# Performance work log

Hardware: AMD Instinct MI355X
Metric: run time of the kernel (lower is better)

The kernel has to match this reference:

```python
import jax, jax.numpy as jnp
import numpy as np

MAP_CHANNEL_WEIGHT = 50.0
PATCH = 3  # unfold kernel size and stride (stride == kernel -> non-overlapping)


def setup_inputs() -> dict:
    key = jax.random.key(0)
    k1, k2, k3, k4 = jax.random.split(key, 4)
    style_resp = jax.random.normal(k1, (1, 256, 256, 256), dtype=jnp.float32)
    style_map = jax.random.uniform(k2, (1, 3, 1024, 1024), dtype=jnp.float32)
    output_map = jax.random.uniform(k3, (1, 3, 1024, 1024), dtype=jnp.float32)
    model_resp = jax.random.normal(k4, (1, 256, 256, 256), dtype=jnp.float32)
    return {"style_resp": style_resp, "style_map": style_map,
            "output_map": output_map, "model_resp": model_resp}


def _avg_pool(x, d):
    # x: (N, C, H, W) -> AvgPool2d((d, d)) with default stride = kernel
    n, c, h, w = x.shape
    return x.reshape(n, c, h // d, d, w // d, d).mean(axis=(3, 5))


def _unfold(x):
    # x: (C, H, W) -> (C*3*3, P) matching torch.nn.Unfold((3,3), stride=3)
    # block layout along dim 0 is (C, kh, kw); patches are row-major.
    c, h, w = x.shape
    nh = (h - PATCH) // PATCH + 1
    nw = (w - PATCH) // PATCH + 1
    x = x[:, : nh * PATCH, : nw * PATCH].reshape(c, nh, PATCH, nw, PATCH)
    x = x.transpose(0, 2, 4, 1, 3)  # (C, kh, kw, nh, nw)
    return x.reshape(c * PATCH * PATCH, nh * nw)


def reference(style_resp, style_map, output_map, model_resp):
    # --- init-time precomputation (faithful to __init__) ---
    channel_count = style_resp.shape[0]  # original code uses dim 0 (batch) here
    patch_height = style_resp.shape[2]
    down = style_map.shape[2] // patch_height
    style_map_down = _avg_pool(style_map, down)
    output_map_down = _avg_pool(output_map, down)
    sr = jnp.concatenate(
        [style_resp, MAP_CHANNEL_WEIGHT * style_map_down * channel_count], axis=1)
    style_patches = _unfold(sr[0])                      # (D, P)
    style_norm_inv = 1.0 / jnp.linalg.norm(style_patches, axis=0)  # (P,)

    # --- loss(model_response) ---
    img = jnp.concatenate(
        [model_resp, MAP_CHANNEL_WEIGHT * output_map_down * channel_count], axis=1)
    img_patches = _unfold(img[0])                       # (D, P)
    img_norm_inv = 1.0 / jnp.linalg.norm(img_patches, axis=0)      # (P,)

    # Faithful to original: sim = ((img^T @ style) * img_norm[j]).T * style_norm[j]
    # => C[i, j] = <img_j, style_i> * img_norm_inv[i] * style_norm_inv[j]
    sim = jnp.einsum('di,dj->ij', style_patches, img_patches)  # (P, P): <style_i, img_j>
    sim = sim * img_norm_inv[:, None] * style_norm_inv[None, :]
    nearest = jnp.argmax(sim, axis=1)                   # (P,)

    matched = style_patches[:, nearest]                 # (D, P)
    loss = jnp.mean((img_patches - matched) ** 2)
    return loss
```

## Files before the change

### kernel.cpp

```cpp
#include <hip/hip_runtime.h>
#include <float.h>
#include <math.h>

#define D_REAL 2331
#define D_PAD  2336
#define DQ     2304
#define N_REAL 7225
#define N_PAD  7296
#define JTILES 57
#define ITILES 57

typedef __attribute__((ext_vector_type(8))) short bf16x8_t;
typedef __attribute__((ext_vector_type(4))) float f32x4_t;
typedef __attribute__((ext_vector_type(8))) int   v8i_t;
typedef __attribute__((ext_vector_type(4))) int   v4i_t;

__device__ __forceinline__ unsigned short f2bf(float x) {
    union { float f; unsigned int u; } v; v.f = x;
    unsigned int r = v.u + 0x7FFFu + ((v.u >> 16) & 1u);
    return (unsigned short)(r >> 16);
}
__device__ __forceinline__ float bflo(unsigned int u) {
    union { unsigned int x; float f; } v; v.x = u << 16; return v.f;
}
__device__ __forceinline__ float bfhi(unsigned int u) {
    union { unsigned int x; float f; } v; v.x = u & 0xFFFF0000u; return v.f;
}

#define GLOAD_LDS16(g, l) __builtin_amdgcn_global_load_lds( \
    (const __attribute__((address_space(1))) void*)(g),     \
    (__attribute__((address_space(3))) void*)(l), 16, 0, 0)

__global__ __launch_bounds__(256) void build_all(
        const float* __restrict__ respS, const float* __restrict__ respI,
        const float* __restrict__ mapS,  const float* __restrict__ mapI,
        unsigned short* __restrict__ PbS, unsigned short* __restrict__ PbI,
        unsigned char* __restrict__ PqS, unsigned char* __restrict__ PqI) {
    const int mat = blockIdx.y;
    unsigned short* Pb = mat ? PbI : PbS;
    const int bx = blockIdx.x;
    if (bx < 6120) {
        const float* resp = mat ? respI : respS;
        unsigned char* Pq = mat ? PqI : PqS;
        __shared__ float slab[5 * 768];
        const int u  = bx / 72;
        const int d0 = (bx - u * 72) * 32;
        const int c0 = d0 / 9;
        const int cN = (d0 + 31) / 9 - c0 + 1;
        const int total = cN * 768;
        for (int idx = threadIdx.x; idx < total; idx += 256) {
            int cc = idx / 768;
            int rem = idx - cc * 768;
            slab[idx] = resp[(((size_t)(c0 + cc)) << 16) + ((size_t)(3 * u) << 8) + rem];
        }
        __syncthreads();
        const int dl16 = threadIdx.x & 15;
        const int de = d0 + 2 * dl16, dq = de + 1;
        const int ce = de / 9, re = de - ce * 9, pe = re / 3, qe = re - pe * 3;
        const int co = dq / 9, ro = dq - co * 9, po = ro / 3, qo = ro - po * 3;
        const int base_e = (ce - c0) * 768 + pe * 256 + qe;
        const int base_o = (co - c0) * 768 + po * 256 + qo;
        const int v0 = threadIdx.x >> 4;
        for (int v = v0; v < 85; v += 16) {
            float x0 = slab[base_e + 3 * v];
            float x1 = slab[base_o + 3 * v];
            size_t row = (size_t)(u * 85 + v);
            *(unsigned int*)&Pb[row * D_PAD + de] =
                (unsigned int)f2bf(x0) | ((unsigned int)f2bf(x1) << 16);
            int pk = __builtin_amdgcn_cvt_pk_fp8_f32(x0, x1, 0, false);
            *(unsigned short*)&Pq[row * DQ + de] = (unsigned short)pk;
        }
    } else {
        const float* map = mat ? mapI : mapS;
        int t = (bx - 6120) * 256 + threadIdx.x;
        int n = t >> 5, dm = t & 31;
        if (n >= N_REAL) return;
        float val = 0.f;
        if (dm < 27) {
            int u = n / 85, v = n - u * 85;
            int ch = dm / 9, r9 = dm - ch * 9, p = r9 / 3, q = r9 - p * 3;
            const float* mp = map + ((size_t)ch << 20)
                                  + ((size_t)((3 * u + p) * 4) << 10)
                                  + (size_t)((3 * v + q) * 4);
            float s = 0.f;
            #pragma unroll
            for (int a = 0; a < 4; a++)
                #pragma unroll
                for (int b = 0; b < 4; b++) s += mp[a * 1024 + b];
            val = 3.125f * s;
        }
        Pb[(size_t)n * D_PAD + 2304 + dm] = f2bf(val);
    }
}

__global__ __launch_bounds__(256) void col_norms(const unsigned short* __restrict__ Sb,
                                                 float* __restrict__ sinv,
                                                 double* __restrict__ accum) {
    if (blockIdx.x == 0 && threadIdx.x == 0) *accum = 0.0;
    int n = blockIdx.x * 4 + (threadIdx.x >> 6);
    int lane = threadIdx.x & 63;
    const uint4* sp = (const uint4*)(Sb + (size_t)n * D_PAD);
    float s = 0.f;
    for (int k = lane; k < D_PAD / 8; k += 64) {
        uint4 a = sp[k];
        float x0 = bflo(a.x), x1 = bfhi(a.x), x2 = bflo(a.y), x3 = bfhi(a.y);
        float x4 = bflo(a.z), x5 = bfhi(a.z), x6 = bflo(a.w), x7 = bfhi(a.w);
        s = fmaf(x0, x0, s); s = fmaf(x1, x1, s);
        s = fmaf(x2, x2, s); s = fmaf(x3, x3, s);
        s = fmaf(x4, x4, s); s = fmaf(x5, x5, s);
        s = fmaf(x6, x6, s); s = fmaf(x7, x7, s);
    }
    #pragma unroll
    for (int off = 32; off > 0; off >>= 1) s += __shfl_xor(s, off);
    if (lane == 0) sinv[n] = (n < N_REAL) ? rsqrtf(s) : 0.f;
}

__global__ __launch_bounds__(512, 4) void gemm_argmax(
        const unsigned char* __restrict__ Sq, const unsigned char* __restrict__ Iq,
        const unsigned short* __restrict__ Sb, const unsigned short* __restrict__ Ib,
        const float* __restrict__ sinv,
        float* __restrict__ pval, int* __restrict__ pidx) {
    const int bid = blockIdx.x;
    const int it = bid % ITILES, jt = bid / ITILES;
    const int i0 = it * 128, j0 = jt * 128;

    __shared__ __align__(16) unsigned char Af[2][128][128];
    __shared__ __align__(16) unsigned char Bf[2][128][128];

    const int tid = threadIdx.x;
    const int L = tid & 63, w = tid >> 6;
    const int wr = w >> 2, wc = w & 3;
    const int m = L & 15, q = L >> 4;
    const int clo = ((2 * q)     ^ (m & 7)) << 4;
    const int chi = ((2 * q + 1) ^ (m & 7)) << 4;

    f32x4_t acc[4][2];
    #pragma unroll
    for (int a = 0; a < 4; a++)
        #pragma unroll
        for (int b = 0; b < 2; b++) acc[a][b] = (f32x4_t){0.f, 0.f, 0.f, 0.f};

    const int r8 = 8 * w + (L >> 3);
    const int swz = ((L & 7) ^ (L >> 3)) << 4;
    const unsigned char* pA = Sq + (size_t)(i0 + r8 + (r8 & 32)) * DQ + swz;
    const unsigned char* pB = Iq + (size_t)(j0 + r8) * DQ + swz;

#define STG_A(h, ko, b) GLOAD_LDS16(pA + (size_t)(32 * (h)) * DQ + (ko), \
                                    &Af[b][64 * (h) + 8 * w][0])
#define STG_B(h, ko, b) GLOAD_LDS16(pB + (size_t)(64 * (h)) * DQ + (ko), \
                                    &Bf[b][64 * (h) + 8 * w][0])

#define LDA8(dst, b, mi) {                                                    \
    const unsigned char* p_ =                                                 \
        &Af[b][(((mi) >> 1) << 6) + (wr << 5) + (((mi) & 1) << 4) + m][0];    \
    v4i_t lo_ = *(const v4i_t*)(p_ + clo);                                    \
    v4i_t hi_ = *(const v4i_t*)(p_ + chi);                                    \
    dst = __builtin_shufflevector(lo_, hi_, 0, 1, 2, 3, 4, 5, 6, 7); }
#define LDB8(dst, b, nj) {                                                    \
    const unsigned char* p_ = &Bf[b][(wc << 5) + ((nj) << 4) + m][0];         \
    v4i_t lo_ = *(const v4i_t*)(p_ + clo);                                    \
    v4i_t hi_ = *(const v4i_t*)(p_ + chi);                                    \
    dst = __builtin_shufflevector(lo_, hi_, 0, 1, 2, 3, 4, 5, 6, 7); }

#define RDB2(b) LDB8(bq0, b, 0) LDB8(bq1, b, 1)

#define MXMFMA(a, b, c) __builtin_amdgcn_mfma_scale_f32_16x16x128_f8f6f4( \
    a, b, c, 0, 0, 0, 0x7F, 0, 0x7F)

#define GATE3 asm volatile("s_waitcnt vmcnt(3)" ::: "memory");
#define GATE0 asm volatile("s_waitcnt vmcnt(0)" ::: "memory");

#define PHASE(b, h, RDB, STAGES, GATE) {                                \
    v8i_t a0_, a1_;                                                     \
    RDB                                                                 \
    LDA8(a0_, b, 2 * (h))                                               \
    LDA8(a1_, b, 2 * (h) + 1)                                           \
    STAGES                                                              \
    __builtin_amdgcn_sched_barrier(0);                                  \
    __builtin_amdgcn_s_barrier();                                       \
    asm volatile("s_waitcnt lgkmcnt(0)" ::: "memory");                  \
    __builtin_amdgcn_sched_barrier(0);                                  \
    __builtin_amdgcn_s_setprio(1);                                      \
    acc[2*(h)  ][0] = MXMFMA(a0_, bq0, acc[2*(h)  ][0]);                \
    acc[2*(h)  ][1] = MXMFMA(a0_, bq1, acc[2*(h)  ][1]);                \
    acc[2*(h)+1][0] = MXMFMA(a1_, bq0, acc[2*(h)+1][0]);                \
    acc[2*(h)+1][1] = MXMFMA(a1_, bq1, acc[2*(h)+1][1]);                \
    __builtin_amdgcn_s_setprio(0);                                      \
    __builtin_amdgcn_sched_barrier(0);                                  \
    GATE                                                                \
    __builtin_amdgcn_s_barrier();                                       \
}

    v8i_t bq0, bq1;

    STG_B(0, 0, 0); STG_B(1, 0, 0); STG_A(0, 0, 0); STG_A(1, 0, 0);
    STG_B(0, 128, 1); STG_B(1, 128, 1); STG_A(0, 128, 1);
    GATE3
    __builtin_amdgcn_s_barrier();

    #pragma unroll 1
    for (int p = 0; p < 8; ++p) {
        PHASE(0, 0, RDB2(0), STG_A(1, 128, 1);, )
        PHASE(0, 1, ,        STG_B(0, 256, 0); STG_B(1, 256, 0); STG_A(0, 256, 0);, GATE3)
        PHASE(1, 0, RDB2(1), STG_A(1, 256, 0);, )
        PHASE(1, 1, ,        STG_B(0, 384, 1); STG_B(1, 384, 1); STG_A(0, 384, 1);, GATE3)
        pA += 256; pB += 256;
    }

    unsigned short (*At)[32] = (unsigned short(*)[32])&Af[0][0][0];
    unsigned short (*Bt)[32] = (unsigned short(*)[32])&Bf[0][0][0];
    const unsigned short* ptA = Sb + (size_t)(i0 + 16 * w + (L >> 2)) * D_PAD
                              + 2304 + (((L & 3) ^ ((L >> 3) & 3)) << 3);
    const unsigned short* ptB = Ib + (size_t)(j0 + 16 * w + (L >> 2)) * D_PAD
                              + 2304 + (((L & 3) ^ ((L >> 3) & 3)) << 3);

    PHASE(0, 0, RDB2(0), STG_A(1, 128, 1);, )
    PHASE(0, 1, , , GATE0)
    PHASE(1, 0, RDB2(1),
          GLOAD_LDS16(ptA, &At[16 * w][0]);
          GLOAD_LDS16(ptB, &Bt[16 * w][0]);, )
    PHASE(1, 1, , , GATE0)
#undef PHASE
#undef RDB2
#undef STG_A
#undef STG_B

    {
        const int cht = (q ^ ((m >> 1) & 3)) << 3;
        bf16x8_t bt0 = *(const bf16x8_t*)&Bt[(wc << 5) + m][cht];
        bf16x8_t bt1 = *(const bf16x8_t*)&Bt[(wc << 5) + 16 + m][cht];
        #pragma unroll
        for (int mi = 0; mi < 4; mi++) {
            bf16x8_t a_ = *(const bf16x8_t*)&At[(wr << 6) + mi * 16 + m][cht];
            acc[mi][0] = __builtin_amdgcn_mfma_f32_16x16x32_bf16(
                a_, bt0, acc[mi][0], 0, 0, 0);
            acc[mi][1] = __builtin_amdgcn_mfma_f32_16x16x32_bf16(
                a_, bt1, acc[mi][1], 0, 0, 0);
        }
    }

    const float sj0 = sinv[j0 + (wc << 5) + m];
    const float sj1 = sinv[j0 + (wc << 5) + 16 + m];
    #pragma unroll
    for (int mi = 0; mi < 4; mi++) {
        #pragma unroll
        for (int r = 0; r < 4; r++) {
            float best = -INFINITY; int bidx = 0x7fffffff;
            {
                int j = j0 + (wc << 5) + m;
                float v = (j < N_REAL) ? acc[mi][0][r] * sj0 : -INFINITY;
                if (v > best) { best = v; bidx = j; }
                j += 16;
                v = (j < N_REAL) ? acc[mi][1][r] * sj1 : -INFINITY;
                if (v > best) { best = v; bidx = j; }
            }
            #pragma unroll
            for (int off = 1; off < 16; off <<= 1) {
                float ov = __shfl_xor(best, off);
                int   oi = __shfl_xor(bidx, off);
                if (ov > best || (ov == best && oi < bidx)) { best = ov; bidx = oi; }
            }
            if (m == 0) {
                int i = i0 + (wr << 6) + mi * 16 + (q << 2) + r;
                pval[(size_t)jt * N_PAD + i] = best;
                pidx[(size_t)jt * N_PAD + i] = bidx;
            }
        }
    }
}

__global__ __launch_bounds__(256) void loss_kernel(
        const unsigned short* __restrict__ Ib, const unsigned short* __restrict__ Sb,
        const float* __restrict__ pval, const int* __restrict__ pidx,
        double* __restrict__ accum) {
    __shared__ float wsum[4];
    __shared__ int sjn;
    const int n = blockIdx.x;
    if (threadIdx.x < 64) {
        float v = -INFINITY; int id = 0x7fffffff;
        if (threadIdx.x < JTILES) {
            v  = pval[(size_t)threadIdx.x * N_PAD + n];
            id = pidx[(size_t)threadIdx.x * N_PAD + n];
        }
        #pragma unroll
        for (int off = 32; off > 0; off >>= 1) {
            float ov = __shfl_xor(v, off);
            int   oi = __shfl_xor(id, off);
            if (ov > v || (ov == v && oi < id)) { v = ov; id = oi; }
        }
        if (threadIdx.x == 0) sjn = id;
    }
    __syncthreads();
    const int jn = sjn;
    const uint4* ip = (const uint4*)(Ib + (size_t)n  * D_PAD);
    const uint4* sp = (const uint4*)(Sb + (size_t)jn * D_PAD);
    float s = 0.f;
    for (int k = threadIdx.x; k < D_PAD / 8; k += 256) {
        uint4 a = ip[k], b = sp[k];
        float d0 = bflo(a.x) - bflo(b.x), d1 = bfhi(a.x) - bfhi(b.x);
        float d2 = bflo(a.y) - bflo(b.y), d3 = bfhi(a.y) - bfhi(b.y);
        float d4 = bflo(a.z) - bflo(b.z), d5 = bfhi(a.z) - bfhi(b.z);
        float d6 = bflo(a.w) - bflo(b.w), d7 = bfhi(a.w) - bfhi(b.w);
        s = fmaf(d0, d0, s); s = fmaf(d1, d1, s);
        s = fmaf(d2, d2, s); s = fmaf(d3, d3, s);
        s = fmaf(d4, d4, s); s = fmaf(d5, d5, s);
        s = fmaf(d6, d6, s); s = fmaf(d7, d7, s);
    }
    #pragma unroll
    for (int off = 32; off > 0; off >>= 1) s += __shfl_xor(s, off);
    int lane = threadIdx.x & 63, wv = threadIdx.x >> 6;
    if (lane == 0) wsum[wv] = s;
    __syncthreads();
    if (threadIdx.x == 0) {
        double t = (double)wsum[0] + (double)wsum[1] + (double)wsum[2] + (double)wsum[3];
        atomicAdd(accum, t);
    }
}

__global__ void finalize(const double* __restrict__ accum, float* __restrict__ out) {
    out[0] = (float)(accum[0] / (double)((long long)D_REAL * N_REAL));
}

extern "C" void kernel_launch(void* const* d_in, const int* in_sizes, int n_in,
                              void* d_out, int out_size, void* d_ws, size_t ws_size,
                              hipStream_t stream) {
    const float* style_resp = (const float*)d_in[0];
    const float* style_map  = (const float*)d_in[1];
    const float* output_map = (const float*)d_in[2];
    const float* model_resp = (const float*)d_in[3];
    float* out = (float*)d_out;

    unsigned short* Sb = (unsigned short*)d_ws;
    unsigned short* Ib = Sb + (size_t)D_PAD * N_PAD;
    unsigned char*  Sq = (unsigned char*)(Ib + (size_t)D_PAD * N_PAD);
    unsigned char*  Iq = Sq + (size_t)DQ * N_PAD;
    float* sinv    = (float*)(Iq + (size_t)DQ * N_PAD);
    float* pval    = sinv + N_PAD;
    int*   pidx    = (int*)(pval + (size_t)JTILES * N_PAD);
    double* accum  = (double*)(pidx + (size_t)JTILES * N_PAD);

    build_all<<<dim3(6120 + 904, 2), 256, 0, stream>>>(
        style_resp, model_resp, style_map, output_map, Sb, Ib, Sq, Iq);

    col_norms<<<N_PAD / 4, 256, 0, stream>>>(Sb, sinv, accum);

    gemm_argmax<<<ITILES * JTILES, 512, 0, stream>>>(Sq, Iq, Sb, Ib, sinv, pval, pidx);

    loss_kernel<<<N_REAL, 256, 0, stream>>>(Ib, Sb, pval, pidx, accum);
    finalize<<<1, 1, 0, stream>>>(accum, out);
}
```

Before: 498.1 us.

## Enlarge GEMM-argmax tiles to 256x256 with 32x32 scaled FP8 MFMA

The fused FP8 GEMM and argmax kernel moves from 128x128 to 256x256 output tiles and switches from 16x16x128 to 32x32x64 scaled MFMA instructions, with a matching bf16 32x32x16 tail for the last K slice. Each loaded tile is reused across more outputs, which cuts global and LDS traffic per FLOP and halves the number of per-tile argmax partials. In exchange it uses more LDS and registers (occupancy hint drops from 4 to 2), pads N to 7424 so more padding work is wasted, and launches fewer blocks (841), which may leave CUs unevenly loaded.

```diff
diff --git a/kernel.cpp b/kernel.cpp
--- a/kernel.cpp
+++ b/kernel.cpp
@@ -6,12 +6,11 @@
 #define D_PAD  2336
 #define DQ     2304
 #define N_REAL 7225
-#define N_PAD  7296
-#define JTILES 57
-#define ITILES 57
+#define NPI    7424
+#define NTILES 29
 
 typedef __attribute__((ext_vector_type(8))) short bf16x8_t;
-typedef __attribute__((ext_vector_type(4))) float f32x4_t;
+typedef __attribute__((ext_vector_type(16))) float f32x16_t;
 typedef __attribute__((ext_vector_type(8))) int   v8i_t;
 typedef __attribute__((ext_vector_type(4))) int   v4i_t;
 
@@ -115,155 +114,175 @@
     if (lane == 0) sinv[n] = (n < N_REAL) ? rsqrtf(s) : 0.f;
 }
 
-__global__ __launch_bounds__(512, 4) void gemm_argmax(
+__global__ __launch_bounds__(512, 2) void gemm_argmax(
         const unsigned char* __restrict__ Sq, const unsigned char* __restrict__ Iq,
         const unsigned short* __restrict__ Sb, const unsigned short* __restrict__ Ib,
         const float* __restrict__ sinv,
         float* __restrict__ pval, int* __restrict__ pidx) {
     const int bid = blockIdx.x;
-    const int it = bid % ITILES, jt = bid / ITILES;
-    const int i0 = it * 128, j0 = jt * 128;
-
-    __shared__ __align__(16) unsigned char Af[2][128][128];
-    __shared__ __align__(16) unsigned char Bf[2][128][128];
+    const int it = bid % NTILES, jt = bid / NTILES;
+    const int i0 = it * 256, j0 = jt * 256;
+
+    __shared__ __align__(16) unsigned char Af[2][256][128];
+    __shared__ __align__(16) unsigned char Bf[2][256][128];
 
     const int tid = threadIdx.x;
     const int L = tid & 63, w = tid >> 6;
     const int wr = w >> 2, wc = w & 3;
-    const int m = L & 15, q = L >> 4;
-    const int clo = ((2 * q)     ^ (m & 7)) << 4;
-    const int chi = ((2 * q + 1) ^ (m & 7)) << 4;
-
-    f32x4_t acc[4][2];
+
+    f32x16_t acc[4][2];
     #pragma unroll
     for (int a = 0; a < 4; a++)
         #pragma unroll
-        for (int b = 0; b < 2; b++) acc[a][b] = (f32x4_t){0.f, 0.f, 0.f, 0.f};
-
-    const int r8 = 8 * w + (L >> 3);
+        for (int b = 0; b < 2; b++)
+            acc[a][b] = (f32x16_t){0.f,0.f,0.f,0.f,0.f,0.f,0.f,0.f,
+                                   0.f,0.f,0.f,0.f,0.f,0.f,0.f,0.f};
+
     const int swz = ((L & 7) ^ (L >> 3)) << 4;
-    const unsigned char* pA = Sq + (size_t)(i0 + r8 + (r8 & 32)) * DQ + swz;
-    const unsigned char* pB = Iq + (size_t)(j0 + r8) * DQ + swz;
+    const unsigned char* pA = Sq + (size_t)(i0 + (w >> 2) * 128 + 8 * (w & 3) + (L >> 3)) * DQ + swz;
+    const unsigned char* pB = Iq + (size_t)(j0 + 8 * w + (L >> 3)) * DQ + swz;
 
 #define STG_A(h, ko, b) GLOAD_LDS16(pA + (size_t)(32 * (h)) * DQ + (ko), \
-                                    &Af[b][64 * (h) + 8 * w][0])
+                                    &Af[b][((h) << 6) + (w << 3)][0])
 #define STG_B(h, ko, b) GLOAD_LDS16(pB + (size_t)(64 * (h)) * DQ + (ko), \
-                                    &Bf[b][64 * (h) + 8 * w][0])
-
-#define LDA8(dst, b, mi) {                                                    \
-    const unsigned char* p_ =                                                 \
-        &Af[b][(((mi) >> 1) << 6) + (wr << 5) + (((mi) & 1) << 4) + m][0];    \
-    v4i_t lo_ = *(const v4i_t*)(p_ + clo);                                    \
-    v4i_t hi_ = *(const v4i_t*)(p_ + chi);                                    \
+                                    &Bf[b][((h) << 6) + (w << 3)][0])
+
+#define LDFRAG(dst, rowp, kh) {                                               \
+    const unsigned char* p_ = (rowp);                                         \
+    v4i_t lo_ = *(const v4i_t*)(p_ + (((((kh) << 2) + ((L >> 5) << 1)    ) ^ (L & 7)) << 4)); \
+    v4i_t hi_ = *(const v4i_t*)(p_ + (((((kh) << 2) + ((L >> 5) << 1) + 1) ^ (L & 7)) << 4)); \
     dst = __builtin_shufflevector(lo_, hi_, 0, 1, 2, 3, 4, 5, 6, 7); }
-#define LDB8(dst, b, nj) {                                                    \
-    const unsigned char* p_ = &Bf[b][(wc << 5) + ((nj) << 4) + m][0];         \
-    v4i_t lo_ = *(const v4i_t*)(p_ + clo);                                    \
-    v4i_t hi_ = *(const v4i_t*)(p_ + chi);                                    \
-    dst = __builtin_shufflevector(lo_, hi_, 0, 1, 2, 3, 4, 5, 6, 7); }
-
-#define RDB2(b) LDB8(bq0, b, 0) LDB8(bq1, b, 1)
-
-#define MXMFMA(a, b, c) __builtin_amdgcn_mfma_scale_f32_16x16x128_f8f6f4( \
+
+#define AROW(b, mi) (&Af[b][((mi) << 6) + (wr << 5) + (L & 31)][0])
+#define BROW(b, nj) (&Bf[b][(wc << 6) + ((nj) << 5) + (L & 31)][0])
+
+#define RDB(b) LDFRAG(bq0, BROW(b, 0), 0) LDFRAG(bq1, BROW(b, 1), 0) \
+               LDFRAG(bq2, BROW(b, 0), 1) LDFRAG(bq3, BROW(b, 1), 1)
+
+#define MXMFMA(a, b, c) __builtin_amdgcn_mfma_scale_f32_32x32x64_f8f6f4( \
     a, b, c, 0, 0, 0, 0x7F, 0, 0x7F)
 
-#define GATE3 asm volatile("s_waitcnt vmcnt(3)" ::: "memory");
+#define GATE7 asm volatile("s_waitcnt vmcnt(7)" ::: "memory");
+#define GATE4 asm volatile("s_waitcnt vmcnt(4)" ::: "memory");
 #define GATE0 asm volatile("s_waitcnt vmcnt(0)" ::: "memory");
 
-#define PHASE(b, h, RDB, STAGES, GATE) {                                \
+#define PHASE(b, mi, RDB_, STAGES, GATE) {                              \
     v8i_t a0_, a1_;                                                     \
-    RDB                                                                 \
-    LDA8(a0_, b, 2 * (h))                                               \
-    LDA8(a1_, b, 2 * (h) + 1)                                           \
+    RDB_                                                                \
+    LDFRAG(a0_, AROW(b, mi), 0)                                         \
+    LDFRAG(a1_, AROW(b, mi), 1)                                         \
     STAGES                                                              \
     __builtin_amdgcn_sched_barrier(0);                                  \
     __builtin_amdgcn_s_barrier();                                       \
     asm volatile("s_waitcnt lgkmcnt(0)" ::: "memory");                  \
     __builtin_amdgcn_sched_barrier(0);                                  \
     __builtin_amdgcn_s_setprio(1);                                      \
-    acc[2*(h)  ][0] = MXMFMA(a0_, bq0, acc[2*(h)  ][0]);                \
-    acc[2*(h)  ][1] = MXMFMA(a0_, bq1, acc[2*(h)  ][1]);                \
-    acc[2*(h)+1][0] = MXMFMA(a1_, bq0, acc[2*(h)+1][0]);                \
-    acc[2*(h)+1][1] = MXMFMA(a1_, bq1, acc[2*(h)+1][1]);                \
+    acc[mi][0] = MXMFMA(a0_, bq0, acc[mi][0]);                          \
+    acc[mi][1] = MXMFMA(a0_, bq1, acc[mi][1]);                          \
+    acc[mi][0] = MXMFMA(a1_, bq2, acc[mi][0]);                          \
+    acc[mi][1] = MXMFMA(a1_, bq3, acc[mi][1]);                          \
     __builtin_amdgcn_s_setprio(0);                                      \
     __builtin_amdgcn_sched_barrier(0);                                  \
     GATE                                                                \
     __builtin_amdgcn_s_barrier();                                       \
 }
 
-    v8i_t bq0, bq1;
-
-    STG_B(0, 0, 0); STG_B(1, 0, 0); STG_A(0, 0, 0); STG_A(1, 0, 0);
-    STG_B(0, 128, 1); STG_B(1, 128, 1); STG_A(0, 128, 1);
-    GATE3
+    v8i_t bq0, bq1, bq2, bq3;
+
+    STG_B(0, 0, 0); STG_B(1, 0, 0); STG_B(2, 0, 0); STG_B(3, 0, 0);
+    STG_A(0, 0, 0); STG_A(1, 0, 0); STG_A(2, 0, 0); STG_A(3, 0, 0);
+    STG_B(0, 128, 1); STG_B(1, 128, 1); STG_B(2, 128, 1); STG_B(3, 128, 1);
+    STG_A(0, 128, 1); STG_A(1, 128, 1); STG_A(2, 128, 1);
+    GATE7
     __builtin_amdgcn_s_barrier();
 
     #pragma unroll 1
     for (int p = 0; p < 8; ++p) {
-        PHASE(0, 0, RDB2(0), STG_A(1, 128, 1);, )
-        PHASE(0, 1, ,        STG_B(0, 256, 0); STG_B(1, 256, 0); STG_A(0, 256, 0);, GATE3)
-        PHASE(1, 0, RDB2(1), STG_A(1, 256, 0);, )
-        PHASE(1, 1, ,        STG_B(0, 384, 1); STG_B(1, 384, 1); STG_A(0, 384, 1);, GATE3)
+        PHASE(0, 0, RDB(0), STG_A(3, 128, 1);, )
+        PHASE(0, 1, ,       STG_B(0, 256, 0); STG_B(1, 256, 0); STG_A(0, 256, 0);, )
+        PHASE(0, 2, ,       STG_B(2, 256, 0); STG_B(3, 256, 0); STG_A(1, 256, 0);, )
+        PHASE(0, 3, ,       STG_A(2, 256, 0);, GATE7)
+        PHASE(1, 0, RDB(1), STG_A(3, 256, 0);, )
+        PHASE(1, 1, ,       STG_B(0, 384, 1); STG_B(1, 384, 1); STG_A(0, 384, 1);, )
+        PHASE(1, 2, ,       STG_B(2, 384, 1); STG_B(3, 384, 1); STG_A(1, 384, 1);, )
+        PHASE(1, 3, ,       STG_A(2, 384, 1);, GATE7)
         pA += 256; pB += 256;
     }
 
     unsigned short (*At)[32] = (unsigned short(*)[32])&Af[0][0][0];
     unsigned short (*Bt)[32] = (unsigned short(*)[32])&Bf[0][0][0];
     const unsigned short* ptA = Sb + (size_t)(i0 + 16 * w + (L >> 2)) * D_PAD
-                              + 2304 + (((L & 3) ^ ((L >> 3) & 3)) << 3);
+                              + 2304 + (((L & 3) ^ ((L >> 2) & 3)) << 3);
     const unsigned short* ptB = Ib + (size_t)(j0 + 16 * w + (L >> 2)) * D_PAD
-                              + 2304 + (((L & 3) ^ ((L >> 3) & 3)) << 3);
-
-    PHASE(0, 0, RDB2(0), STG_A(1, 128, 1);, )
-    PHASE(0, 1, , , GATE0)
-    PHASE(1, 0, RDB2(1),
-          GLOAD_LDS16(ptA, &At[16 * w][0]);
-          GLOAD_LDS16(ptB, &Bt[16 * w][0]);, )
-    PHASE(1, 1, , , GATE0)
+                              + 2304 + (((L & 3) ^ ((L >> 2) & 3)) << 3);
+#define TSTG_A(h) GLOAD_LDS16(ptA + (size_t)((h) * 128) * D_PAD, &At[((h) << 7) + (w << 4)][0]);
+#define TSTG_B(h) GLOAD_LDS16(ptB + (size_t)((h) * 128) * D_PAD, &Bt[((h) << 7) + (w << 4)][0]);
+
+    PHASE(0, 0, RDB(0), STG_A(3, 128, 1);, )
+    PHASE(0, 1, ,       TSTG_A(0) TSTG_B(0), )
+    PHASE(0, 2, ,       TSTG_A(1) TSTG_B(1), )
+    PHASE(0, 3, , , GATE4)
+    PHASE(1, 0, RDB(1), , )
+    PHASE(1, 1, , , )
+    PHASE(1, 2, , , )
+    PHASE(1, 3, , , GATE0)
 #undef PHASE
-#undef RDB2
+#undef RDB
 #undef STG_A
 #undef STG_B
+#undef TSTG_A
+#undef TSTG_B
 
     {
-        const int cht = (q ^ ((m >> 1) & 3)) << 3;
-        bf16x8_t bt0 = *(const bf16x8_t*)&Bt[(wc << 5) + m][cht];
-        bf16x8_t bt1 = *(const bf16x8_t*)&Bt[(wc << 5) + 16 + m][cht];
+        bf16x8_t bt[2][2];
+        #pragma unroll
+        for (int kt = 0; kt < 2; kt++)
+            #pragma unroll
+            for (int nj = 0; nj < 2; nj++) {
+                int row = (wc << 6) + (nj << 5) + (L & 31);
+                bt[kt][nj] = *(const bf16x8_t*)
+                    &Bt[row][((2 * kt + (L >> 5)) ^ (L & 3)) << 3];
+            }
         #pragma unroll
         for (int mi = 0; mi < 4; mi++) {
-            bf16x8_t a_ = *(const bf16x8_t*)&At[(wr << 6) + mi * 16 + m][cht];
-            acc[mi][0] = __builtin_amdgcn_mfma_f32_16x16x32_bf16(
-                a_, bt0, acc[mi][0], 0, 0, 0);
-            acc[mi][1] = __builtin_amdgcn_mfma_f32_16x16x32_bf16(
-                a_, bt1, acc[mi][1], 0, 0, 0);
-        }
-    }
-
-    const float sj0 = sinv[j0 + (wc << 5) + m];
-    const float sj1 = sinv[j0 + (wc << 5) + 16 + m];
+            int row = (wr << 7) + (mi << 5) + (L & 31);
+            #pragma unroll
+            for (int kt = 0; kt < 2; kt++) {
+                bf16x8_t a_ = *(const bf16x8_t*)
+                    &At[row][((2 * kt + (L >> 5)) ^ (L & 3)) << 3];
+                acc[mi][0] = __builtin_amdgcn_mfma_f32_32x32x16_bf16(
+                    a_, bt[kt][0], acc[mi][0], 0, 0, 0);
+                acc[mi][1] = __builtin_amdgcn_mfma_f32_32x32x16_bf16(
+                    a_, bt[kt][1], acc[mi][1], 0, 0, 0);
+            }
+        }
+    }
+
+    const int jb = j0 + (wc << 6) + (L & 31);
+    const float sj0 = sinv[jb], sj1 = sinv[jb + 32];
     #pragma unroll
     for (int mi = 0; mi < 4; mi++) {
         #pragma unroll
-        for (int r = 0; r < 4; r++) {
+        for (int r = 0; r < 16; r++) {
             float best = -INFINITY; int bidx = 0x7fffffff;
             {
-                int j = j0 + (wc << 5) + m;
-                float v = (j < N_REAL) ? acc[mi][0][r] * sj0 : -INFINITY;
-                if (v > best) { best = v; bidx = j; }
-                j += 16;
-                v = (j < N_REAL) ? acc[mi][1][r] * sj1 : -INFINITY;
-                if (v > best) { best = v; bidx = j; }
+                float v = (jb < N_REAL) ? acc[mi][0][r] * sj0 : -INFINITY;
+                if (v > best) { best = v; bidx = jb; }
+                int j1 = jb + 32;
+                v = (j1 < N_REAL) ? acc[mi][1][r] * sj1 : -INFINITY;
+                if (v > best) { best = v; bidx = j1; }
             }
             #pragma unroll
-            for (int off = 1; off < 16; off <<= 1) {
+            for (int off = 1; off < 32; off <<= 1) {
                 float ov = __shfl_xor(best, off);
                 int   oi = __shfl_xor(bidx, off);
                 if (ov > best || (ov == best && oi < bidx)) { best = ov; bidx = oi; }
             }
-            if (m == 0) {
-                int i = i0 + (wr << 6) + mi * 16 + (q << 2) + r;
-                pval[(size_t)jt * N_PAD + i] = best;
-                pidx[(size_t)jt * N_PAD + i] = bidx;
+            if ((L & 31) == 0) {
+                int i = i0 + (wr << 7) + (mi << 5) + ((L >> 5) << 2)
+                      + (r & 3) + ((r >> 2) << 3);
+                pval[(size_t)jt * NPI + i] = best;
+                pidx[(size_t)jt * NPI + i] = bidx;
             }
         }
     }
@@ -278,9 +297,9 @@
     const int n = blockIdx.x;
     if (threadIdx.x < 64) {
         float v = -INFINITY; int id = 0x7fffffff;
-        if (threadIdx.x < JTILES) {
-            v  = pval[(size_t)threadIdx.x * N_PAD + n];
-            id = pidx[(size_t)threadIdx.x * N_PAD + n];
+        if (threadIdx.x < NTILES) {
+            v  = pval[(size_t)threadIdx.x * NPI + n];
+            id = pidx[(size_t)threadIdx.x * NPI + n];
         }
         #pragma unroll
         for (int off = 32; off > 0; off >>= 1) {
@@ -331,20 +350,20 @@
     float* out = (float*)d_out;
 
     unsigned short* Sb = (unsigned short*)d_ws;
-    unsigned short* Ib = Sb + (size_t)D_PAD * N_PAD;
-    unsigned char*  Sq = (unsigned char*)(Ib + (size_t)D_PAD * N_PAD);
-    unsigned char*  Iq = Sq + (size_t)DQ * N_PAD;
-    float* sinv    = (float*)(Iq + (size_t)DQ * N_PAD);
-    float* pval    = sinv + N_PAD;
-    int*   pidx    = (int*)(pval + (size_t)JTILES * N_PAD);
-    double* accum  = (double*)(pidx + (size_t)JTILES * N_PAD);
+    unsigned short* Ib = Sb + (size_t)D_PAD * NPI;
+    unsigned char*  Sq = (unsigned char*)(Ib + (size_t)D_PAD * NPI);
+    unsigned char*  Iq = Sq + (size_t)DQ * NPI;
+    float* sinv    = (float*)(Iq + (size_t)DQ * NPI);
+    float* pval    = sinv + NPI;
+    int*   pidx    = (int*)(pval + (size_t)NTILES * NPI);
+    double* accum  = (double*)(pidx + (size_t)NTILES * NPI);
 
     build_all<<<dim3(6120 + 904, 2), 256, 0, stream>>>(
         style_resp, model_resp, style_map, output_map, Sb, Ib, Sq, Iq);
 
-    col_norms<<<N_PAD / 4, 256, 0, stream>>>(Sb, sinv, accum);
-
-    gemm_argmax<<<ITILES * JTILES, 512, 0, stream>>>(Sq, Iq, Sb, Ib, sinv, pval, pidx);
+    col_norms<<<NPI / 4, 256, 0, stream>>>(Sb, sinv, accum);
+
+    gemm_argmax<<<NTILES * NTILES, 512, 0, stream>>>(Sq, Iq, Sb, Ib, sinv, pval, pidx);
 
     loss_kernel<<<N_REAL, 256, 0, stream>>>(Ib, Sb, pval, pidx, accum);
     finalize<<<1, 1, 0, stream>>>(accum, out);
```

Measured after the change: 559.3 us. 12.3% more time.
